# Optimization experiments

Measured on AMD Instinct MI355X. Metric: run time of the kernel, lower is better.

The kernel has to match this reference:

```python
import jax, jax.numpy as jnp
import numpy as np

B, C, H, W = 1, 256, 64, 64
K_DIM, V_DIM, HEADS = 64, 64, 8


def setup_inputs() -> dict:
    key = jax.random.key(0)
    ks = jax.random.split(key, 13)
    s = lambda i, shape: jax.random.normal(ks[i], shape, dtype=jnp.float32) * 0.05
    return {
        "x": s(0, (B, C, H, W)),
        # low-rank bottleneck projections (bias=False), torch Linear weight is [out,in]
        "wq1": s(1, (K_DIM // 2, C)),
        "wk1": s(2, (K_DIM // 2, C)),
        "wv1": s(3, (V_DIM // 2, C)),
        # expansion to per-head dims (bias=False)
        "wq2": s(4, (K_DIM * HEADS, K_DIM // 2)),
        "wk2": s(5, (K_DIM * HEADS, K_DIM // 2)),
        "wv2": s(6, (V_DIM * HEADS, V_DIM // 2)),
        # output projection (with bias)
        "wo": s(7, (C, V_DIM * HEADS)),
        "bo": s(8, (C,)),
        # depthwise 3x3 conv (groups=C): [C,1,3,3]
        "w_dw": s(9, (C, 1, 3, 3)),
        "b_dw": s(10, (C,)),
        # 1x1 gate conv
        "w_gate": s(11, (C, C, 1, 1)),
        "b_gate": s(12, (C,)),
    }


def reference(x, wq1, wk1, wv1, wq2, wk2, wv2, wo, bo, w_dw, b_dw, w_gate, b_gate):
    B_, C_, H_, W_ = x.shape
    N = H_ * W_
    t = x.transpose(0, 2, 3, 1).reshape(B_, N, C_)  # [B, N, C]
    # low-rank then expansion: Linear(x) = x @ W.T
    q = (t @ wq1.T) @ wq2.T  # [B, N, HEADS*K_DIM]
    k = (t @ wk1.T) @ wk2.T
    v = (t @ wv1.T) @ wv2.T
    q = q.reshape(B_, N, HEADS, K_DIM).transpose(0, 2, 1, 3)  # [B,h,N,dk]
    k = k.reshape(B_, N, HEADS, K_DIM).transpose(0, 2, 1, 3)
    v = v.reshape(B_, N, HEADS, V_DIM).transpose(0, 2, 1, 3)
    attn = jnp.einsum('bhnd,bhmd->bhnm', q, k) / jnp.sqrt(jnp.float32(K_DIM))
    attn = jax.nn.softmax(attn, axis=-1)
    out = jnp.einsum('bhnm,bhmd->bhnd', attn, v)  # [B,h,N,dv]
    out = out.transpose(0, 2, 1, 3).reshape(B_, N, HEADS * V_DIM)
    out = out @ wo.T + bo  # [B, N, C]
    out = out.reshape(B_, H_, W_, C_).transpose(0, 3, 1, 2)  # NCHW
    dn = ('NCHW', 'OIHW', 'NCHW')
    out = jax.lax.conv_general_dilated(out, w_dw, (1, 1), 'SAME', dimension_numbers=dn,
                                       feature_group_count=C_) + b_dw[None, :, None, None]
    gate = jax.nn.sigmoid(
        jax.lax.conv_general_dilated(out, w_gate, (1, 1), 'SAME', dimension_numbers=dn)
        + b_gate[None, :, None, None])
    return out * gate
```

## Files before the change

### kernel.cpp

```cpp
#include <hip/hip_runtime.h>

typedef __bf16 bf16;
typedef __bf16 bf16x4 __attribute__((ext_vector_type(4)));
typedef __bf16 bf16x8 __attribute__((ext_vector_type(8)));
typedef float f32x4 __attribute__((ext_vector_type(4)));

#define MFMA16(a, b, c) __builtin_amdgcn_mfma_f32_16x16x32_bf16((a), (b), (c), 0, 0, 0)

__device__ inline float fexp2(float x) {
    float r;
    asm("v_exp_f32 %0, %1" : "=v"(r) : "v"(x));
    return r;
}

__global__ void k_pre(const float* __restrict__ x, bf16* __restrict__ xt,
                      const float* __restrict__ wq1, const float* __restrict__ wk1,
                      const float* __restrict__ wv1, const float* __restrict__ wq2,
                      const float* __restrict__ wk2, const float* __restrict__ wv2,
                      const float* __restrict__ wo, const float* __restrict__ wg,
                      bf16* __restrict__ Wq, bf16* __restrict__ Wk, bf16* __restrict__ Wv,
                      bf16* __restrict__ wo_bf, bf16* __restrict__ wg_bf) {
    __shared__ float tile[64][68];
    const int bx = blockIdx.x;
    if (bx < 256) {
        const int t = threadIdx.x;
        const int c0 = (bx & 3) * 64;
        const int n0 = (bx >> 2) * 64;
        {
            const int cr = t >> 4, nc = (t & 15) * 4;
#pragma unroll
            for (int i = 0; i < 4; ++i) {
                const float4 v = *(const float4*)(x + (size_t)(c0 + cr + i * 16) * 4096 + n0 + nc);
                tile[cr + i * 16][nc + 0] = v.x;
                tile[cr + i * 16][nc + 1] = v.y;
                tile[cr + i * 16][nc + 2] = v.z;
                tile[cr + i * 16][nc + 3] = v.w;
            }
        }
        __syncthreads();
        const int n = t >> 2, cc = (t & 3) * 16;
        bf16x8 o0, o1;
#pragma unroll
        for (int j = 0; j < 8; ++j) o0[j] = (bf16)tile[cc + j][n];
#pragma unroll
        for (int j = 0; j < 8; ++j) o1[j] = (bf16)tile[cc + 8 + j][n];
        bf16* dst = xt + (size_t)(n0 + n) * 256 + c0 + cc;
        *(bf16x8*)dst = o0;
        *(bf16x8*)(dst + 8) = o1;
    } else {
        int t = (bx - 256) * 256 + threadIdx.x;
        if (t < 393216) {
            int which = t >> 17;
            int rem = t & 131071;
            int o = rem >> 8, c = rem & 255;
            const float* w1 = which == 0 ? wq1 : which == 1 ? wk1 : wv1;
            const float* w2 = which == 0 ? wq2 : which == 1 ? wk2 : wv2;
            float acc = 0.f;
#pragma unroll
            for (int j = 0; j < 32; ++j) acc += w2[o * 32 + j] * w1[j * 256 + c];
            bf16* W = which == 0 ? Wq : which == 1 ? Wk : Wv;
            W[o * 256 + c] = (bf16)acc;
        } else if (t < 524288) {
            int idx = t - 393216;
            wo_bf[idx] = (bf16)wo[idx];
        } else if (t < 589824) {
            int idx = t - 524288;
            wg_bf[idx] = (bf16)wg[idx];
        }
    }
}

template <int MODE>
__launch_bounds__(256)
__global__ void k_gemm_nt(const bf16* __restrict__ A, const bf16* __restrict__ B,
                          int K, float scale, void* __restrict__ outp,
                          const float* __restrict__ bias, const float* __restrict__ mul) {
    const int lane = threadIdx.x & 63;
    const int w = threadIdx.x >> 6;
    const int i0 = blockIdx.y * 128 + w * 32;
    const int j0 = blockIdx.x * 64;
    const int lrow = lane & 15;
    const int lk = (lane >> 4) * 8;

    f32x4 acc[2][4];
#pragma unroll
    for (int a = 0; a < 2; ++a)
#pragma unroll
        for (int b = 0; b < 4; ++b) acc[a][b] = (f32x4){0.f, 0.f, 0.f, 0.f};

    for (int k0 = 0; k0 < K; k0 += 32) {
        bf16x8 af[2], bfr[4];
#pragma unroll
        for (int qs = 0; qs < 2; ++qs)
            af[qs] = *(const bf16x8*)(A + (size_t)(i0 + qs * 16 + lrow) * K + k0 + lk);
#pragma unroll
        for (int js = 0; js < 4; ++js)
            bfr[js] = *(const bf16x8*)(B + (size_t)(j0 + js * 16 + lrow) * K + k0 + lk);
#pragma unroll
        for (int qs = 0; qs < 2; ++qs)
#pragma unroll
            for (int js = 0; js < 4; ++js)
                acc[qs][js] = MFMA16(af[qs], bfr[js], acc[qs][js]);
    }

    const int rbase = (lane >> 4) * 4;
#pragma unroll
    for (int qs = 0; qs < 2; ++qs)
#pragma unroll
        for (int js = 0; js < 4; ++js)
#pragma unroll
            for (int r = 0; r < 4; ++r) {
                int i = i0 + qs * 16 + rbase + r;
                int j = j0 + js * 16 + lrow;
                float v = acc[qs][js][r];
                if (MODE == 0) {
                    ((bf16*)outp)[(size_t)(j >> 6) * (4096 * 64) + (size_t)i * 64 + (j & 63)] =
                        (bf16)(v * scale);
                } else if (MODE == 1) {
                    ((bf16*)outp)[(size_t)i * 4096 + j] = (bf16)v;
                } else if (MODE == 2) {
                    ((float*)outp)[(size_t)i * 4096 + j] = v + bias[i];
                } else {
                    float g = v + bias[i];
                    float sg = 1.f / (1.f + __expf(-g));
                    ((float*)outp)[(size_t)i * 4096 + j] = mul[(size_t)i * 4096 + j] * sg;
                }
            }
}

__launch_bounds__(256)
__global__ void k_attn(const bf16* __restrict__ q, const bf16* __restrict__ k,
                       const bf16* __restrict__ vT, bf16* __restrict__ Opart,
                       float* __restrict__ lpart) {
    __shared__ char kvlds[2][16384];
    __shared__ char plds[4][4096];
    const int tid = threadIdx.x;
    const int lane = tid & 63;
    const int w = tid >> 6;
    const int split = blockIdx.x >> 8;
    const int h = (blockIdx.x >> 5) & 7;
    const int qt = blockIdx.x & 31;
    const int qbase = qt * 128 + w * 32;
    const int lrow = lane & 15;
    const int g = lane >> 4;
    const int swzr = (lrow & 7) << 4;

    const bf16* qh = q + (size_t)h * 4096 * 64;
    const bf16* kh = k + (size_t)h * 4096 * 64;
    const bf16* vh = vT + (size_t)h * 64 * 4096;
    char* myp = plds[w];

    const int isV = tid >> 7;
    const int srow = (tid & 127) >> 1;
    const int shalf = tid & 1;
    const int swzs = (srow & 7) << 4;
    const int ldoff = isV * 8192 + srow * 128;
    const bf16* sbase = isV ? (vh + (size_t)srow * 4096 + split * 1024 + shalf * 32)
                            : (kh + ((size_t)split * 1024 + srow) * 64 + shalf * 32);
    const size_t sstep = isV ? 64 : 64 * 64;

    bf16x8 bq[2][2];
#pragma unroll
    for (int qs = 0; qs < 2; ++qs)
#pragma unroll
        for (int ks = 0; ks < 2; ++ks)
            bq[qs][ks] = *(const bf16x8*)(qh + (size_t)(qbase + qs * 16 + lrow) * 64 +
                                          ks * 32 + g * 8);

    f32x4 accO[2][4];
    f32x4 l_acc[2];
#pragma unroll
    for (int qs = 0; qs < 2; ++qs) {
#pragma unroll
        for (int ds = 0; ds < 4; ++ds) accO[qs][ds] = (f32x4){0.f, 0.f, 0.f, 0.f};
        l_acc[qs] = (f32x4){0.f, 0.f, 0.f, 0.f};
    }
    bf16x8 ones;
#pragma unroll
    for (int i = 0; i < 8; ++i) ones[i] = (bf16)1.0f;

    uint4 r0, r1, r2, r3;
    {
        const bf16* p = sbase;
        r0 = *(const uint4*)(p);
        r1 = *(const uint4*)(p + 8);
        r2 = *(const uint4*)(p + 16);
        r3 = *(const uint4*)(p + 24);
    }
    {
        char* d = kvlds[0] + ldoff;
        *(uint4*)(d + ((shalf * 64 + 0) ^ swzs)) = r0;
        *(uint4*)(d + ((shalf * 64 + 16) ^ swzs)) = r1;
        *(uint4*)(d + ((shalf * 64 + 32) ^ swzs)) = r2;
        *(uint4*)(d + ((shalf * 64 + 48) ^ swzs)) = r3;
    }
    {
        const bf16* p = sbase + sstep;
        r0 = *(const uint4*)(p);
        r1 = *(const uint4*)(p + 8);
        r2 = *(const uint4*)(p + 16);
        r3 = *(const uint4*)(p + 24);
    }
    __syncthreads();

    for (int t = 0; t < 16; ++t) {
        const int cur = t & 1;
        if (t < 15) {
            char* d = kvlds[cur ^ 1] + ldoff;
            *(uint4*)(d + ((shalf * 64 + 0) ^ swzs)) = r0;
            *(uint4*)(d + ((shalf * 64 + 16) ^ swzs)) = r1;
            *(uint4*)(d + ((shalf * 64 + 32) ^ swzs)) = r2;
            *(uint4*)(d + ((shalf * 64 + 48) ^ swzs)) = r3;
        }
        if (t < 14) {
            const bf16* p = sbase + (size_t)(t + 2) * sstep;
            r0 = *(const uint4*)(p);
            r1 = *(const uint4*)(p + 8);
            r2 = *(const uint4*)(p + 16);
            r3 = *(const uint4*)(p + 24);
        }
        const char* Kl = kvlds[cur];
        const char* Vl = kvlds[cur] + 8192;

#pragma unroll
        for (int qs = 0; qs < 2; ++qs) {
            const int qrow = qs * 16 + lrow;
            f32x4 s[4];
#pragma unroll
            for (int js = 0; js < 4; ++js) s[js] = (f32x4){0.f, 0.f, 0.f, 0.f};
#pragma unroll
            for (int ks = 0; ks < 2; ++ks) {
                bf16x8 ak[4];
#pragma unroll
                for (int js = 0; js < 4; ++js)
                    ak[js] = *(const bf16x8*)(Kl + (js * 16 + lrow) * 128 +
                                              ((ks * 64 + g * 16) ^ swzr));
#pragma unroll
                for (int js = 0; js < 4; ++js)
                    s[js] = MFMA16(ak[js], bq[qs][ks], s[js]);
            }
#pragma unroll
            for (int js = 0; js < 4; ++js) {
                bf16x4 pk;
#pragma unroll
                for (int r = 0; r < 4; ++r) pk[r] = (bf16)fexp2(s[js][r]);
                *(bf16x4*)(myp + ((qrow * 128 + js * 32 + g * 8) ^ swzr)) = pk;
            }
#pragma unroll
            for (int ks2 = 0; ks2 < 2; ++ks2) {
                bf16x8 ap = *(const bf16x8*)(myp + ((qrow * 128 + ks2 * 64 + g * 16) ^ swzr));
                bf16x8 bv[4];
#pragma unroll
                for (int ds = 0; ds < 4; ++ds)
                    bv[ds] = *(const bf16x8*)(Vl + (ds * 16 + lrow) * 128 +
                                              ((ks2 * 64 + g * 16) ^ swzr));
#pragma unroll
                for (int ds = 0; ds < 4; ++ds)
                    accO[qs][ds] = MFMA16(ap, bv[ds], accO[qs][ds]);
                l_acc[qs] = MFMA16(ap, ones, l_acc[qs]);
            }
        }
        __syncthreads();
    }

#pragma unroll
    for (int qs = 0; qs < 2; ++qs)
#pragma unroll
        for (int ds = 0; ds < 4; ++ds)
#pragma unroll
            for (int r = 0; r < 4; ++r) {
                const int n = qbase + qs * 16 + 4 * g + r;
                Opart[((size_t)split * 4096 + n) * 512 + h * 64 + ds * 16 + lrow] =
                    (bf16)accO[qs][ds][r];
            }
    if (lrow == 0) {
#pragma unroll
        for (int qs = 0; qs < 2; ++qs)
#pragma unroll
            for (int r = 0; r < 4; ++r)
                lpart[((size_t)split * 8 + h) * 4096 + qbase + qs * 16 + 4 * g + r] =
                    l_acc[qs][r];
    }
}

__global__ void k_combine(const bf16* __restrict__ Opart, const float* __restrict__ lpart,
                          bf16* __restrict__ o) {
    const int tid = blockIdx.x * 256 + threadIdx.x;
    const int n = tid >> 6;
    const int c8 = (tid & 63) * 8;
    const int h = c8 >> 6;
    float acc[8] = {0, 0, 0, 0, 0, 0, 0, 0};
    float l = 0.f;
#pragma unroll
    for (int s = 0; s < 4; ++s) {
        const bf16x8 v = *(const bf16x8*)(Opart + ((size_t)s * 4096 + n) * 512 + c8);
#pragma unroll
        for (int j = 0; j < 8; ++j) acc[j] += (float)v[j];
        l += lpart[((size_t)s * 8 + h) * 4096 + n];
    }
    const float inv = 1.f / l;
    bf16x8 ov;
#pragma unroll
    for (int j = 0; j < 8; ++j) ov[j] = (bf16)(acc[j] * inv);
    *(bf16x8*)(o + (size_t)n * 512 + c8) = ov;
}

__global__ void k_dw(const float* __restrict__ y, const float* __restrict__ wdw,
                     const float* __restrict__ bdw, float* __restrict__ dwout,
                     bf16* __restrict__ dwt) {
    int t = blockIdx.x * 256 + threadIdx.x;
    int c = t >> 12, n = t & 4095, yy = n >> 6, xx = n & 63;
    float acc = bdw[c];
    const float* yc = y + (size_t)c * 4096;
#pragma unroll
    for (int ky = 0; ky < 3; ++ky) {
        int ry = yy + ky - 1;
        if ((unsigned)ry < 64u) {
#pragma unroll
            for (int kx = 0; kx < 3; ++kx) {
                int rx = xx + kx - 1;
                if ((unsigned)rx < 64u) acc += wdw[c * 9 + ky * 3 + kx] * yc[ry * 64 + rx];
            }
        }
    }
    dwout[t] = acc;
    dwt[n * 256 + c] = (bf16)acc;
}

extern "C" void kernel_launch(void* const* d_in, const int* in_sizes, int n_in,
                              void* d_out, int out_size, void* d_ws, size_t ws_size,
                              hipStream_t stream) {
    const float* x   = (const float*)d_in[0];
    const float* wq1 = (const float*)d_in[1];
    const float* wk1 = (const float*)d_in[2];
    const float* wv1 = (const float*)d_in[3];
    const float* wq2 = (const float*)d_in[4];
    const float* wk2 = (const float*)d_in[5];
    const float* wv2 = (const float*)d_in[6];
    const float* wo  = (const float*)d_in[7];
    const float* bo  = (const float*)d_in[8];
    const float* wdw = (const float*)d_in[9];
    const float* bdw = (const float*)d_in[10];
    const float* wg  = (const float*)d_in[11];
    const float* bg  = (const float*)d_in[12];

    char* ws = (char*)d_ws;
    size_t off = 0;
    auto alloc = [&](size_t bytes) {
        char* p = ws + off;
        off += (bytes + 255) & ~(size_t)255;
        return p;
    };
    bf16*  q_buf = (bf16*)alloc((size_t)8 * 4096 * 64 * 2);
    bf16*  k_buf = (bf16*)alloc((size_t)8 * 4096 * 64 * 2);
    bf16*  vT    = (bf16*)alloc((size_t)8 * 64 * 4096 * 2);
    bf16*  o_buf = (bf16*)alloc((size_t)4096 * 512 * 2);
    bf16*  wo_bf = (bf16*)alloc((size_t)256 * 512 * 2);
    bf16*  wg_bf = (bf16*)alloc((size_t)256 * 256 * 2);
    char* U = ws + off;
    bf16*  xbf = (bf16*)U;
    bf16*  Wq  = (bf16*)(U + (size_t)2 * 1024 * 1024);
    bf16*  Wk  = (bf16*)(U + (size_t)2 * 1024 * 1024 + 262144);
    bf16*  Wv  = (bf16*)(U + (size_t)2 * 1024 * 1024 + 524288);
    bf16*  Opart = (bf16*)U;
    float* lpart = (float*)(U + (size_t)16 * 1024 * 1024);
    float* ybuf  = (float*)U;
    float* dwout = (float*)(U + (size_t)4 * 1024 * 1024);
    bf16*  dwt   = (bf16*)(U + (size_t)8 * 1024 * 1024);
    (void)ws_size; (void)in_sizes; (void)n_in; (void)out_size;

    const float QSCALE = 0.125f * 1.4426950408889634f;

    k_pre<<<2560, 256, 0, stream>>>(x, xbf, wq1, wk1, wv1, wq2, wk2, wv2, wo, wg,
                                    Wq, Wk, Wv, wo_bf, wg_bf);
    k_gemm_nt<0><<<dim3(8, 32), 256, 0, stream>>>(xbf, Wq, 256, QSCALE, q_buf, nullptr, nullptr);
    k_gemm_nt<0><<<dim3(8, 32), 256, 0, stream>>>(xbf, Wk, 256, 1.0f, k_buf, nullptr, nullptr);
    k_gemm_nt<1><<<dim3(64, 4), 256, 0, stream>>>(Wv, xbf, 256, 1.0f, vT, nullptr, nullptr);
    k_attn<<<1024, 256, 0, stream>>>(q_buf, k_buf, vT, Opart, lpart);
    k_combine<<<1024, 256, 0, stream>>>(Opart, lpart, o_buf);
    k_gemm_nt<2><<<dim3(64, 2), 256, 0, stream>>>(wo_bf, o_buf, 512, 1.0f, ybuf, bo, nullptr);
    k_dw<<<4096, 256, 0, stream>>>(ybuf, wdw, bdw, dwout, dwt);
    k_gemm_nt<3><<<dim3(64, 2), 256, 0, stream>>>(wg_bf, dwt, 256, 1.0f, d_out, bg, dwout);
}
```

Before: 127.0 us.

## Merge QKV GEMM launches and single-buffer attention K/V tile with setprio

The three Q/K/V projection GEMMs are merged into one 768-block launch, which removes two kernel launches and lets the three projections run concurrently. The attention kernel drops its LDS double buffer for a single K/V tile. Each iteration now stores registers to LDS, prefetches the next tile into registers, and synchronises before compute. That halves the K/V LDS footprint, which may raise occupancy, but it adds a barrier per iteration and reduces load/compute overlap. s_setprio hints are placed around the MFMA sections to favour matrix-issuing waves.

```diff
diff --git a/kernel.cpp b/kernel.cpp
--- a/kernel.cpp
+++ b/kernel.cpp
@@ -71,14 +71,14 @@
 }
 
 template <int MODE>
-__launch_bounds__(256)
-__global__ void k_gemm_nt(const bf16* __restrict__ A, const bf16* __restrict__ B,
-                          int K, float scale, void* __restrict__ outp,
-                          const float* __restrict__ bias, const float* __restrict__ mul) {
+__device__ __forceinline__ void gemm_body(const bf16* __restrict__ A, const bf16* __restrict__ B,
+                                          int K, float scale, void* __restrict__ outp,
+                                          const float* __restrict__ bias,
+                                          const float* __restrict__ mul, int bx, int by) {
     const int lane = threadIdx.x & 63;
     const int w = threadIdx.x >> 6;
-    const int i0 = blockIdx.y * 128 + w * 32;
-    const int j0 = blockIdx.x * 64;
+    const int i0 = by * 128 + w * 32;
+    const int j0 = bx * 64;
     const int lrow = lane & 15;
     const int lk = (lane >> 4) * 8;
 
@@ -128,11 +128,36 @@
             }
 }
 
+template <int MODE>
+__launch_bounds__(256)
+__global__ void k_gemm_nt(const bf16* __restrict__ A, const bf16* __restrict__ B,
+                          int K, float scale, void* __restrict__ outp,
+                          const float* __restrict__ bias, const float* __restrict__ mul) {
+    gemm_body<MODE>(A, B, K, scale, outp, bias, mul, blockIdx.x, blockIdx.y);
+}
+
+__launch_bounds__(256)
+__global__ void k_qkv(const bf16* __restrict__ xbf, const bf16* __restrict__ Wq,
+                      const bf16* __restrict__ Wk, const bf16* __restrict__ Wv,
+                      bf16* __restrict__ q_buf, bf16* __restrict__ k_buf,
+                      bf16* __restrict__ vT, float qscale) {
+    const int b = blockIdx.x;
+    if (b < 256) {
+        gemm_body<0>(xbf, Wq, 256, qscale, q_buf, nullptr, nullptr, b & 7, b >> 3);
+    } else if (b < 512) {
+        const int bb = b - 256;
+        gemm_body<0>(xbf, Wk, 256, 1.0f, k_buf, nullptr, nullptr, bb & 7, bb >> 3);
+    } else {
+        const int bb = b - 512;
+        gemm_body<1>(Wv, xbf, 256, 1.0f, vT, nullptr, nullptr, bb & 63, bb >> 6);
+    }
+}
+
 __launch_bounds__(256)
 __global__ void k_attn(const bf16* __restrict__ q, const bf16* __restrict__ k,
                        const bf16* __restrict__ vT, bf16* __restrict__ Opart,
                        float* __restrict__ lpart) {
-    __shared__ char kvlds[2][16384];
+    __shared__ char kvlds[16384];
     __shared__ char plds[4][4096];
     const int tid = threadIdx.x;
     const int lane = tid & 63;
@@ -149,12 +174,14 @@
     const bf16* kh = k + (size_t)h * 4096 * 64;
     const bf16* vh = vT + (size_t)h * 64 * 4096;
     char* myp = plds[w];
+    const char* Kl = kvlds;
+    const char* Vl = kvlds + 8192;
 
     const int isV = tid >> 7;
     const int srow = (tid & 127) >> 1;
     const int shalf = tid & 1;
     const int swzs = (srow & 7) << 4;
-    const int ldoff = isV * 8192 + srow * 128;
+    char* ldst = kvlds + isV * 8192 + srow * 128;
     const bf16* sbase = isV ? (vh + (size_t)srow * 4096 + split * 1024 + shalf * 32)
                             : (kh + ((size_t)split * 1024 + srow) * 64 + shalf * 32);
     const size_t sstep = isV ? 64 : 64 * 64;
@@ -187,40 +214,20 @@
         r2 = *(const uint4*)(p + 16);
         r3 = *(const uint4*)(p + 24);
     }
-    {
-        char* d = kvlds[0] + ldoff;
-        *(uint4*)(d + ((shalf * 64 + 0) ^ swzs)) = r0;
-        *(uint4*)(d + ((shalf * 64 + 16) ^ swzs)) = r1;
-        *(uint4*)(d + ((shalf * 64 + 32) ^ swzs)) = r2;
-        *(uint4*)(d + ((shalf * 64 + 48) ^ swzs)) = r3;
-    }
-    {
-        const bf16* p = sbase + sstep;
-        r0 = *(const uint4*)(p);
-        r1 = *(const uint4*)(p + 8);
-        r2 = *(const uint4*)(p + 16);
-        r3 = *(const uint4*)(p + 24);
-    }
-    __syncthreads();
 
     for (int t = 0; t < 16; ++t) {
-        const int cur = t & 1;
+        *(uint4*)(ldst + ((shalf * 64 + 0) ^ swzs)) = r0;
+        *(uint4*)(ldst + ((shalf * 64 + 16) ^ swzs)) = r1;
+        *(uint4*)(ldst + ((shalf * 64 + 32) ^ swzs)) = r2;
+        *(uint4*)(ldst + ((shalf * 64 + 48) ^ swzs)) = r3;
         if (t < 15) {
-            char* d = kvlds[cur ^ 1] + ldoff;
-            *(uint4*)(d + ((shalf * 64 + 0) ^ swzs)) = r0;
-            *(uint4*)(d + ((shalf * 64 + 16) ^ swzs)) = r1;
-            *(uint4*)(d + ((shalf * 64 + 32) ^ swzs)) = r2;
-            *(uint4*)(d + ((shalf * 64 + 48) ^ swzs)) = r3;
-        }
-        if (t < 14) {
-            const bf16* p = sbase + (size_t)(t + 2) * sstep;
+            const bf16* p = sbase + (size_t)(t + 1) * sstep;
             r0 = *(const uint4*)(p);
             r1 = *(const uint4*)(p + 8);
             r2 = *(const uint4*)(p + 16);
             r3 = *(const uint4*)(p + 24);
         }
-        const char* Kl = kvlds[cur];
-        const char* Vl = kvlds[cur] + 8192;
+        __syncthreads();
 
 #pragma unroll
         for (int qs = 0; qs < 2; ++qs) {
@@ -228,6 +235,7 @@
             f32x4 s[4];
 #pragma unroll
             for (int js = 0; js < 4; ++js) s[js] = (f32x4){0.f, 0.f, 0.f, 0.f};
+            __builtin_amdgcn_s_setprio(1);
 #pragma unroll
             for (int ks = 0; ks < 2; ++ks) {
                 bf16x8 ak[4];
@@ -239,6 +247,7 @@
                 for (int js = 0; js < 4; ++js)
                     s[js] = MFMA16(ak[js], bq[qs][ks], s[js]);
             }
+            __builtin_amdgcn_s_setprio(0);
 #pragma unroll
             for (int js = 0; js < 4; ++js) {
                 bf16x4 pk;
@@ -246,6 +255,7 @@
                 for (int r = 0; r < 4; ++r) pk[r] = (bf16)fexp2(s[js][r]);
                 *(bf16x4*)(myp + ((qrow * 128 + js * 32 + g * 8) ^ swzr)) = pk;
             }
+            __builtin_amdgcn_s_setprio(1);
 #pragma unroll
             for (int ks2 = 0; ks2 < 2; ++ks2) {
                 bf16x8 ap = *(const bf16x8*)(myp + ((qrow * 128 + ks2 * 64 + g * 16) ^ swzr));
@@ -259,6 +269,7 @@
                     accO[qs][ds] = MFMA16(ap, bv[ds], accO[qs][ds]);
                 l_acc[qs] = MFMA16(ap, ones, l_acc[qs]);
             }
+            __builtin_amdgcn_s_setprio(0);
         }
         __syncthreads();
     }
@@ -373,9 +384,7 @@
 
     k_pre<<<2560, 256, 0, stream>>>(x, xbf, wq1, wk1, wv1, wq2, wk2, wv2, wo, wg,
                                     Wq, Wk, Wv, wo_bf, wg_bf);
-    k_gemm_nt<0><<<dim3(8, 32), 256, 0, stream>>>(xbf, Wq, 256, QSCALE, q_buf, nullptr, nullptr);
-    k_gemm_nt<0><<<dim3(8, 32), 256, 0, stream>>>(xbf, Wk, 256, 1.0f, k_buf, nullptr, nullptr);
-    k_gemm_nt<1><<<dim3(64, 4), 256, 0, stream>>>(Wv, xbf, 256, 1.0f, vT, nullptr, nullptr);
+    k_qkv<<<768, 256, 0, stream>>>(xbf, Wq, Wk, Wv, q_buf, k_buf, vT, QSCALE);
     k_attn<<<1024, 256, 0, stream>>>(q_buf, k_buf, vT, Opart, lpart);
     k_combine<<<1024, 256, 0, stream>>>(Opart, lpart, o_buf);
     k_gemm_nt<2><<<dim3(64, 2), 256, 0, stream>>>(wo_bf, o_buf, 512, 1.0f, ybuf, bo, nullptr);
```

Result: faster. 121.6 us (-4.3%).
